# Performance work log

Hardware: AMD Instinct MI355X
Metric: run time of the kernel (lower is better)

Reference implementation:

```python
import jax, jax.numpy as jnp
import numpy as np

N = 100000
K = 27  # 3^3 kernel offsets for dimension=3
EPS = 1e-6


def layer_norm(x, gamma, beta):
    mu = jnp.mean(x, axis=-1, keepdims=True)
    var = jnp.mean(jnp.square(x - mu), axis=-1, keepdims=True)
    return (x - mu) * jax.lax.rsqrt(var + EPS) * gamma + beta


def sparse_conv3(x, idx, mask, W):
    # gather-GEMM-scatter form of Minkowski sparse conv:
    # x: [N, Cin], idx/mask: [N, K], W: [K, Cin, Cout]
    xg = jnp.where(mask[..., None], x[idx], 0.0)  # [N, K, Cin]
    return jnp.einsum('nkc,kcd->nd', xg, W)


def setup_inputs() -> dict:
    key = jax.random.key(0)
    ks = jax.random.split(key, 6)
    x = jax.random.normal(ks[0], (N, 32), dtype=jnp.float32)
    neighbor_idx = jax.random.randint(ks[1], (N, K), 0, N, dtype=jnp.int32)
    neighbor_mask = jax.random.randint(ks[2], (N, K), 0, 2) > 0
    W_conv = jax.random.normal(ks[3], (32, 32), dtype=jnp.float32) * 0.1
    W1 = jax.random.normal(ks[4], (K, 32, 128), dtype=jnp.float32) * 0.05
    W2 = jax.random.normal(ks[5], (K, 128, 32), dtype=jnp.float32) * 0.05
    return {
        'x': x,
        'neighbor_idx': neighbor_idx,
        'neighbor_mask': neighbor_mask,
        'W_conv': W_conv,
        'gamma0': jnp.ones((32,), jnp.float32),
        'beta0': jnp.zeros((32,), jnp.float32),
        'W1': W1,
        'gamma1': jnp.ones((128,), jnp.float32),
        'beta1': jnp.zeros((128,), jnp.float32),
        'W2': W2,
        'gamma2': jnp.ones((32,), jnp.float32),
        'beta2': jnp.zeros((32,), jnp.float32),
    }


def reference(x, neighbor_idx, neighbor_mask, W_conv, gamma0, beta0,
              W1, gamma1, beta1, W2, gamma2, beta2):
    gelu = lambda t: jax.nn.gelu(t, approximate=False)  # torch default (erf)
    residual = x
    out = x @ W_conv                      # kernel_size=1 conv == dense matmul
    out = gelu(layer_norm(out, gamma0, beta0))
    out = sparse_conv3(out, neighbor_idx, neighbor_mask, W1)
    out = gelu(layer_norm(out, gamma1, beta1))
    out = sparse_conv3(out, neighbor_idx, neighbor_mask, W2)
    out = layer_norm(out, gamma2, beta2)
    out = out + residual
    return gelu(out)
```

## Files before the change

kernel.cpp:

```cpp
#include <hip/hip_runtime.h>
#include <hip/hip_bf16.h>
#include <math.h>

#define NPTS 100000
#define KOFF 27

typedef __attribute__((ext_vector_type(8))) __bf16 bf16x8;
typedef __attribute__((ext_vector_type(4))) float f32x4;

__device__ __forceinline__ unsigned short f2bf(float f) {
    unsigned int u = __float_as_uint(f);
    u += 0x7fffu + ((u >> 16) & 1u);
    return (unsigned short)(u >> 16);
}

__device__ __forceinline__ float gelu_erf(float v) {
    return 0.5f * v * (1.0f + erff(v * 0.70710678118654752f));
}

__global__ __launch_bounds__(256)
void repack_kernel(const float* __restrict__ W1, const float* __restrict__ W2,
                   const void* __restrict__ maskp,
                   unsigned short* __restrict__ W1p,
                   unsigned short* __restrict__ W2p,
                   int* __restrict__ flagp) {
    int o = blockIdx.x * 256 + threadIdx.x;
    if (o == 0) {
        const unsigned int* mw = (const unsigned int*)maskp;
        int f = 0;
        for (int i = 0; i < 64; ++i) f |= (mw[i] > 1u) ? 1 : 0;
        *flagp = f;
    }
    if (o < KOFF * 32 * 128) {
        int j = o & 7, lane = (o >> 3) & 63;
        int quad = lane >> 4, nn = lane & 15;
        int ct1 = (o >> 9) & 7, k1 = o >> 12;
        int kk1 = quad * 8 + j;
        W1p[o] = f2bf(W1[(k1 * 32 + kk1) * 128 + (ct1 * 16 + nn)]);
        int ct2 = (o >> 9) & 1, kc2 = (o >> 10) & 3, k2 = o >> 12;
        int kk2 = kc2 * 32 + quad * 8 + j;
        W2p[o] = f2bf(W2[(k2 * 128 + kk2) * 32 + (ct2 * 16 + nn)]);
    }
}

__global__ __launch_bounds__(256)
void conv1_ln_gelu(const float* __restrict__ x, const float* __restrict__ Wc,
                   const float* __restrict__ g0, const float* __restrict__ b0,
                   unsigned short* __restrict__ out0) {
    __shared__ float xs[256];
    __shared__ float wc[1024];
    int t = threadIdx.x;
    int nb = blockIdx.x * 8;
    xs[t] = x[nb * 32 + t];
    for (int i = t; i < 1024; i += 256) wc[i] = Wc[i];
    __syncthreads();
    int r = t >> 5, d = t & 31;
    const float* xr = &xs[r * 32];
    float v = 0.f;
#pragma unroll
    for (int c = 0; c < 32; ++c) v = fmaf(xr[c], wc[c * 32 + d], v);
    float s = v, s2 = v * v;
#pragma unroll
    for (int m = 16; m >= 1; m >>= 1) {
        s  += __shfl_xor(s,  m, 32);
        s2 += __shfl_xor(s2, m, 32);
    }
    float mu  = s * (1.f / 32.f);
    float var = s2 * (1.f / 32.f) - mu * mu;
    float y = (v - mu) * rsqrtf(var + 1e-6f) * g0[d] + b0[d];
    out0[nb * 32 + t] = f2bf(gelu_erf(y));
}

__device__ __forceinline__ void stage_gidx64(int* s_gidx, const int* nidx,
                                             const void* maskp, int mflag,
                                             int nb, int t) {
    int cnt = (NPTS - nb < 64 ? NPTS - nb : 64) * KOFF;
    for (int i = t; i < 64 * KOFF; i += 64) {
        int g = -1;
        if (i < cnt) {
            int gi = nidx[nb * KOFF + i];
            int m = mflag ? (int)((const unsigned char*)maskp)[nb * KOFF + i]
                          : ((const int*)maskp)[nb * KOFF + i];
            g = m ? gi : -1;
        }
        s_gidx[i] = g;
    }
}

__global__ __launch_bounds__(64, 2)
void conv_k1(const int* __restrict__ nidx, const void* __restrict__ maskp,
             const int* __restrict__ flagp,
             const unsigned short* __restrict__ out0,
             const unsigned short* __restrict__ W1p,
             const float* __restrict__ g1, const float* __restrict__ b1,
             unsigned short* __restrict__ out1) {
    __shared__ int s_gidx[64 * KOFF];

    int t = threadIdx.x;
    int nb = blockIdx.x * 64;
    int mflag = *flagp;
    stage_gidx64(s_gidx, nidx, maskp, mflag, nb, t);
    __syncthreads();

    int lane = t & 63;
    int mrow = lane & 15, quad = lane >> 4;
    const unsigned short* a_base = out0 + quad * 8;
    const int* gp0 = &s_gidx[(0 * 16 + mrow) * KOFF];
    const int* gp1 = &s_gidx[(1 * 16 + mrow) * KOFF];
    const int* gp2 = &s_gidx[(2 * 16 + mrow) * KOFF];
    const int* gp3 = &s_gidx[(3 * 16 + mrow) * KOFF];

    f32x4 acc[4][8] = {};
    bf16x8 a[2][4], b[2][8];

    {
        const unsigned short* wb = W1p + (lane << 3);
#pragma unroll
        for (int ct = 0; ct < 8; ++ct)
            b[0][ct] = *reinterpret_cast<const bf16x8*>(wb + ((ct * 64) << 3));
        int g0 = gp0[0], g1i = gp1[0], g2 = gp2[0], g3 = gp3[0];
        a[0][0] = bf16x8{}; if (g0  >= 0) a[0][0] = *reinterpret_cast<const bf16x8*>(a_base + g0  * 32);
        a[0][1] = bf16x8{}; if (g1i >= 0) a[0][1] = *reinterpret_cast<const bf16x8*>(a_base + g1i * 32);
        a[0][2] = bf16x8{}; if (g2  >= 0) a[0][2] = *reinterpret_cast<const bf16x8*>(a_base + g2  * 32);
        a[0][3] = bf16x8{}; if (g3  >= 0) a[0][3] = *reinterpret_cast<const bf16x8*>(a_base + g3  * 32);
    }

#pragma unroll
    for (int k = 0; k < KOFF; ++k) {
        int cur = k & 1, nxt = cur ^ 1;
        if (k + 1 < KOFF) {
            const unsigned short* wb = W1p + ((((k + 1) * 8) * 64 + lane) << 3);
#pragma unroll
            for (int ct = 0; ct < 8; ++ct)
                b[nxt][ct] = *reinterpret_cast<const bf16x8*>(wb + ((ct * 64) << 3));
            int g0 = gp0[k + 1], g1i = gp1[k + 1], g2 = gp2[k + 1], g3 = gp3[k + 1];
            a[nxt][0] = bf16x8{}; if (g0  >= 0) a[nxt][0] = *reinterpret_cast<const bf16x8*>(a_base + g0  * 32);
            a[nxt][1] = bf16x8{}; if (g1i >= 0) a[nxt][1] = *reinterpret_cast<const bf16x8*>(a_base + g1i * 32);
            a[nxt][2] = bf16x8{}; if (g2  >= 0) a[nxt][2] = *reinterpret_cast<const bf16x8*>(a_base + g2  * 32);
            a[nxt][3] = bf16x8{}; if (g3  >= 0) a[nxt][3] = *reinterpret_cast<const bf16x8*>(a_base + g3  * 32);
        }
#pragma unroll
        for (int rt = 0; rt < 4; ++rt)
#pragma unroll
            for (int ct = 0; ct < 8; ++ct)
                acc[rt][ct] = __builtin_amdgcn_mfma_f32_16x16x32_bf16(a[cur][rt], b[cur][ct], acc[rt][ct], 0, 0, 0);
    }

    float gv[8], bv[8];
#pragma unroll
    for (int ct = 0; ct < 8; ++ct) {
        gv[ct] = g1[ct * 16 + mrow];
        bv[ct] = b1[ct * 16 + mrow];
    }
#pragma unroll
    for (int rt = 0; rt < 4; ++rt) {
        int n_base = nb + rt * 16 + quad * 4;
#pragma unroll
        for (int r = 0; r < 4; ++r) {
            float s = 0.f, s2 = 0.f;
#pragma unroll
            for (int ct = 0; ct < 8; ++ct) { float v = acc[rt][ct][r]; s += v; s2 += v * v; }
#pragma unroll
            for (int m = 1; m <= 8; m <<= 1) {
                s  += __shfl_xor(s,  m, 16);
                s2 += __shfl_xor(s2, m, 16);
            }
            float mu = s * (1.f / 128.f);
            float rs = rsqrtf(s2 * (1.f / 128.f) - mu * mu + 1e-6f);
            int n = n_base + r;
            if (n < NPTS) {
#pragma unroll
                for (int ct = 0; ct < 8; ++ct) {
                    float y = (acc[rt][ct][r] - mu) * rs * gv[ct] + bv[ct];
                    out1[n * 128 + ct * 16 + mrow] = f2bf(gelu_erf(y));
                }
            }
        }
    }
}

__global__ __launch_bounds__(64, 2)
void conv_k2(const int* __restrict__ nidx, const void* __restrict__ maskp,
             const int* __restrict__ flagp,
             const unsigned short* __restrict__ out1,
             const unsigned short* __restrict__ W2p,
             const float* __restrict__ g2, const float* __restrict__ b2,
             const float* __restrict__ x, float* __restrict__ outp) {
    __shared__ int s_gidx[64 * KOFF];

    int t = threadIdx.x;
    int nb = blockIdx.x * 64;
    int mflag = *flagp;
    stage_gidx64(s_gidx, nidx, maskp, mflag, nb, t);
    __syncthreads();

    int lane = t & 63;
    int mrow = lane & 15, quad = lane >> 4;
    const unsigned short* a_base = out1 + quad * 8;
    const int* gp0 = &s_gidx[(0 * 16 + mrow) * KOFF];
    const int* gp1 = &s_gidx[(1 * 16 + mrow) * KOFF];
    const int* gp2 = &s_gidx[(2 * 16 + mrow) * KOFF];
    const int* gp3 = &s_gidx[(3 * 16 + mrow) * KOFF];

    f32x4 acc[4][2] = {};
    bf16x8 a[2][4][4], b[2][8];

    {
        const unsigned short* wb = W2p + (lane << 3);
#pragma unroll
        for (int f = 0; f < 8; ++f)
            b[0][f] = *reinterpret_cast<const bf16x8*>(wb + ((f * 64) << 3));
        int gg[4] = { gp0[0], gp1[0], gp2[0], gp3[0] };
#pragma unroll
        for (int rt = 0; rt < 4; ++rt) {
#pragma unroll
            for (int kc = 0; kc < 4; ++kc) a[0][rt][kc] = bf16x8{};
            if (gg[rt] >= 0) {
#pragma unroll
                for (int kc = 0; kc < 4; ++kc)
                    a[0][rt][kc] = *reinterpret_cast<const bf16x8*>(a_base + gg[rt] * 128 + kc * 32);
            }
        }
    }

#pragma unroll
    for (int k = 0; k < KOFF; ++k) {
        int cur = k & 1, nxt = cur ^ 1;
        if (k + 1 < KOFF) {
            const unsigned short* wb = W2p + ((((k + 1) * 8) * 64 + lane) << 3);
#pragma unroll
            for (int f = 0; f < 8; ++f)
                b[nxt][f] = *reinterpret_cast<const bf16x8*>(wb + ((f * 64) << 3));
            int gg[4] = { gp0[k + 1], gp1[k + 1], gp2[k + 1], gp3[k + 1] };
#pragma unroll
            for (int rt = 0; rt < 4; ++rt) {
#pragma unroll
                for (int kc = 0; kc < 4; ++kc) a[nxt][rt][kc] = bf16x8{};
                if (gg[rt] >= 0) {
#pragma unroll
                    for (int kc = 0; kc < 4; ++kc)
                        a[nxt][rt][kc] = *reinterpret_cast<const bf16x8*>(a_base + gg[rt] * 128 + kc * 32);
                }
            }
        }
#pragma unroll
        for (int rt = 0; rt < 4; ++rt)
#pragma unroll
            for (int kc = 0; kc < 4; ++kc) {
                acc[rt][0] = __builtin_amdgcn_mfma_f32_16x16x32_bf16(a[cur][rt][kc], b[cur][kc * 2 + 0], acc[rt][0], 0, 0, 0);
                acc[rt][1] = __builtin_amdgcn_mfma_f32_16x16x32_bf16(a[cur][rt][kc], b[cur][kc * 2 + 1], acc[rt][1], 0, 0, 0);
            }
    }

    float gv0 = g2[mrow], gv1 = g2[mrow + 16];
    float bv0 = b2[mrow], bv1 = b2[mrow + 16];
#pragma unroll
    for (int rt = 0; rt < 4; ++rt) {
        int n_base = nb + rt * 16 + quad * 4;
#pragma unroll
        for (int r = 0; r < 4; ++r) {
            float v0 = acc[rt][0][r], v1 = acc[rt][1][r];
            float s = v0 + v1, s2 = v0 * v0 + v1 * v1;
#pragma unroll
            for (int m = 1; m <= 8; m <<= 1) {
                s  += __shfl_xor(s,  m, 16);
                s2 += __shfl_xor(s2, m, 16);
            }
            float mu = s * (1.f / 32.f);
            float rs = rsqrtf(s2 * (1.f / 32.f) - mu * mu + 1e-6f);
            int n = n_base + r;
            if (n < NPTS) {
                float y0 = (v0 - mu) * rs * gv0 + bv0 + x[n * 32 + mrow];
                float y1 = (v1 - mu) * rs * gv1 + bv1 + x[n * 32 + mrow + 16];
                outp[n * 32 + mrow]      = gelu_erf(y0);
                outp[n * 32 + mrow + 16] = gelu_erf(y1);
            }
        }
    }
}

extern "C" void kernel_launch(void* const* d_in, const int* in_sizes, int n_in,
                              void* d_out, int out_size, void* d_ws, size_t ws_size,
                              hipStream_t stream) {
    const float* x    = (const float*)d_in[0];
    const int*   nidx = (const int*)d_in[1];
    const void*  maskp = d_in[2];
    const float* Wc = (const float*)d_in[3];
    const float* g0 = (const float*)d_in[4];
    const float* b0 = (const float*)d_in[5];
    const float* W1 = (const float*)d_in[6];
    const float* g1 = (const float*)d_in[7];
    const float* b1 = (const float*)d_in[8];
    const float* W2 = (const float*)d_in[9];
    const float* g2 = (const float*)d_in[10];
    const float* b2 = (const float*)d_in[11];

    char* ws = (char*)d_ws;
    unsigned short* out0 = (unsigned short*)ws;
    unsigned short* out1 = (unsigned short*)(ws + 6400000);
    unsigned short* W1p  = (unsigned short*)(ws + 32000000);
    unsigned short* W2p  = W1p + KOFF * 32 * 128;
    int* flagp = (int*)(W2p + KOFF * 128 * 32);

    repack_kernel<<<432, 256, 0, stream>>>(W1, W2, maskp, W1p, W2p, flagp);
    conv1_ln_gelu<<<NPTS / 8, 256, 0, stream>>>(x, Wc, g0, b0, out0);
    conv_k1<<<(NPTS + 63) / 64, 64, 0, stream>>>(nidx, maskp, flagp, out0, W1p, g1, b1, out1);
    conv_k2<<<(NPTS + 63) / 64, 64, 0, stream>>>(nidx, maskp, flagp, out1, W2p, g2, b2, x, (float*)d_out);
}
```

Baseline: 276.9 us.

## Stage conv_k2 gathered rows through LDS with compacted coalesced neighbor loads

conv_k2 now builds, per kernel offset, a compacted list of valid neighbor indices. Each neighbor's 256-byte row is fetched cooperatively by 16 lanes as contiguous 16-byte loads into a padded, double-buffered LDS staging area. MFMA A-fragments are then read from LDS through a per-row slot byte, and masked rows point to a zeroed slot. This aims to coalesce the random row gathers and skip loads for masked neighbors. The cost is extra LDS, setup passes and barriers, and the launch-bounds occupancy hint is dropped. There is no synchronisation between the LDS staging writes and the reads of other lanes, which is only safe because a single-wave block runs in lockstep.

```diff
diff --git a/kernel.cpp b/kernel.cpp
--- a/kernel.cpp
+++ b/kernel.cpp
@@ -7,6 +7,7 @@
 
 typedef __attribute__((ext_vector_type(8))) __bf16 bf16x8;
 typedef __attribute__((ext_vector_type(4))) float f32x4;
+typedef __attribute__((ext_vector_type(4))) int i32x4;
 
 __device__ __forceinline__ unsigned short f2bf(float f) {
     unsigned int u = __float_as_uint(f);
@@ -179,7 +180,10 @@
     }
 }
 
-__global__ __launch_bounds__(64, 2)
+#define SLOT_STRIDE 272
+#define BUF_SZ (65 * SLOT_STRIDE)
+
+__global__ __launch_bounds__(64)
 void conv_k2(const int* __restrict__ nidx, const void* __restrict__ maskp,
              const int* __restrict__ flagp,
              const unsigned short* __restrict__ out1,
@@ -187,69 +191,95 @@
              const float* __restrict__ g2, const float* __restrict__ b2,
              const float* __restrict__ x, float* __restrict__ outp) {
     __shared__ int s_gidx[64 * KOFF];
+    __shared__ int glist[KOFF][64];
+    __shared__ unsigned char sbyte[KOFF][64];
+    __shared__ unsigned int cpb[KOFF][16];
+    __shared__ __align__(16) char stage[2 * BUF_SZ];
 
     int t = threadIdx.x;
     int nb = blockIdx.x * 64;
     int mflag = *flagp;
+
     stage_gidx64(s_gidx, nidx, maskp, mflag, nb, t);
-    __syncthreads();
-
-    int lane = t & 63;
-    int mrow = lane & 15, quad = lane >> 4;
-    const unsigned short* a_base = out1 + quad * 8;
-    const int* gp0 = &s_gidx[(0 * 16 + mrow) * KOFF];
-    const int* gp1 = &s_gidx[(1 * 16 + mrow) * KOFF];
-    const int* gp2 = &s_gidx[(2 * 16 + mrow) * KOFF];
-    const int* gp3 = &s_gidx[(3 * 16 + mrow) * KOFF];
-
+    if (t < 34) {
+        int buf = (t >= 17) ? 1 : 0, c = (t >= 17) ? t - 17 : t;
+        *reinterpret_cast<i32x4*>(stage + buf * BUF_SZ + 64 * SLOT_STRIDE + c * 16) = i32x4{0, 0, 0, 0};
+    }
+    __syncthreads();
+
+    if (t < KOFF) {
+        int c = 0;
+        for (int r = 0; r < 64; ++r) {
+            int g = s_gidx[r * KOFF + t];
+            unsigned char sb = 64;
+            if (g >= 0) { sb = (unsigned char)c; glist[t][c] = g; ++c; }
+            sbyte[t][r] = sb;
+        }
+        for (int p = c; p < 64; ++p) glist[t][p] = 0;
+    }
+    __syncthreads();
+    for (int i = t; i < KOFF * 16; i += 64) {
+        int k = i >> 4, mr = i & 15;
+        cpb[k][mr] = (unsigned)sbyte[k][mr]
+                   | ((unsigned)sbyte[k][16 + mr] << 8)
+                   | ((unsigned)sbyte[k][32 + mr] << 16)
+                   | ((unsigned)sbyte[k][48 + mr] << 24);
+    }
+    __syncthreads();
+
+    int mrow = t & 15, quad = t >> 4;
+    int sub = t >> 4, q = t & 15;
     f32x4 acc[4][2] = {};
-    bf16x8 a[2][4][4], b[2][8];
+    i32x4 sreg[16];
+    bf16x8 breg[2][8];
 
     {
-        const unsigned short* wb = W2p + (lane << 3);
+#pragma unroll
+        for (int j = 0; j < 16; ++j) {
+            int g = glist[0][4 * j + sub];
+            sreg[j] = *reinterpret_cast<const i32x4*>(out1 + (size_t)g * 128 + q * 8);
+        }
+        const unsigned short* wb = W2p + (t << 3);
 #pragma unroll
         for (int f = 0; f < 8; ++f)
-            b[0][f] = *reinterpret_cast<const bf16x8*>(wb + ((f * 64) << 3));
-        int gg[4] = { gp0[0], gp1[0], gp2[0], gp3[0] };
-#pragma unroll
-        for (int rt = 0; rt < 4; ++rt) {
-#pragma unroll
-            for (int kc = 0; kc < 4; ++kc) a[0][rt][kc] = bf16x8{};
-            if (gg[rt] >= 0) {
-#pragma unroll
-                for (int kc = 0; kc < 4; ++kc)
-                    a[0][rt][kc] = *reinterpret_cast<const bf16x8*>(a_base + gg[rt] * 128 + kc * 32);
-            }
-        }
+            breg[0][f] = *reinterpret_cast<const bf16x8*>(wb + ((f * 64) << 3));
+#pragma unroll
+        for (int j = 0; j < 16; ++j)
+            *reinterpret_cast<i32x4*>(stage + (4 * j + sub) * SLOT_STRIDE + q * 16) = sreg[j];
     }
 
 #pragma unroll
     for (int k = 0; k < KOFF; ++k) {
         int cur = k & 1, nxt = cur ^ 1;
         if (k + 1 < KOFF) {
-            const unsigned short* wb = W2p + ((((k + 1) * 8) * 64 + lane) << 3);
+#pragma unroll
+            for (int j = 0; j < 16; ++j) {
+                int g = glist[k + 1][4 * j + sub];
+                sreg[j] = *reinterpret_cast<const i32x4*>(out1 + (size_t)g * 128 + q * 8);
+            }
+            const unsigned short* wb = W2p + ((((k + 1) * 8) * 64 + t) << 3);
 #pragma unroll
             for (int f = 0; f < 8; ++f)
-                b[nxt][f] = *reinterpret_cast<const bf16x8*>(wb + ((f * 64) << 3));
-            int gg[4] = { gp0[k + 1], gp1[k + 1], gp2[k + 1], gp3[k + 1] };
-#pragma unroll
-            for (int rt = 0; rt < 4; ++rt) {
-#pragma unroll
-                for (int kc = 0; kc < 4; ++kc) a[nxt][rt][kc] = bf16x8{};
-                if (gg[rt] >= 0) {
-#pragma unroll
-                    for (int kc = 0; kc < 4; ++kc)
-                        a[nxt][rt][kc] = *reinterpret_cast<const bf16x8*>(a_base + gg[rt] * 128 + kc * 32);
-                }
-            }
-        }
-#pragma unroll
-        for (int rt = 0; rt < 4; ++rt)
+                breg[nxt][f] = *reinterpret_cast<const bf16x8*>(wb + ((f * 64) << 3));
+        }
+        unsigned wm = cpb[k][mrow];
+        const char* base = stage + cur * BUF_SZ + quad * 16;
+#pragma unroll
+        for (int rt = 0; rt < 4; ++rt) {
+            int s = (wm >> (8 * rt)) & 255;
+            const char* rowb = base + s * SLOT_STRIDE;
 #pragma unroll
             for (int kc = 0; kc < 4; ++kc) {
-                acc[rt][0] = __builtin_amdgcn_mfma_f32_16x16x32_bf16(a[cur][rt][kc], b[cur][kc * 2 + 0], acc[rt][0], 0, 0, 0);
-                acc[rt][1] = __builtin_amdgcn_mfma_f32_16x16x32_bf16(a[cur][rt][kc], b[cur][kc * 2 + 1], acc[rt][1], 0, 0, 0);
-            }
+                bf16x8 af = *reinterpret_cast<const bf16x8*>(rowb + kc * 64);
+                acc[rt][0] = __builtin_amdgcn_mfma_f32_16x16x32_bf16(af, breg[cur][kc * 2 + 0], acc[rt][0], 0, 0, 0);
+                acc[rt][1] = __builtin_amdgcn_mfma_f32_16x16x32_bf16(af, breg[cur][kc * 2 + 1], acc[rt][1], 0, 0, 0);
+            }
+        }
+        if (k + 1 < KOFF) {
+#pragma unroll
+            for (int j = 0; j < 16; ++j)
+                *reinterpret_cast<i32x4*>(stage + nxt * BUF_SZ + (4 * j + sub) * SLOT_STRIDE + q * 16) = sreg[j];
+        }
     }
 
     float gv0 = g2[mrow], gv1 = g2[mrow + 16];
```

After: 520.8 us. 88.1% more time.

## Split sparse conv blocks across two waves and deepen gather prefetch

Applied to the files above, without the earlier changes.

Both sparse-conv kernels now launch 128 threads per 64-point block, with each wave owning 32 rows instead of one wave owning all 64. This halves per-wave accumulator and A-fragment registers so more waves can fit per CU, at the cost of each wave reloading the full weight slice. conv_k1 also gets a triple-buffered gather that prefetches two offsets ahead, and conv_k2 issues the gather loads before the weight loads. The index-staging loop now strides by 128 so the two waves share that work.

```diff
diff --git a/kernel.cpp b/kernel.cpp
--- a/kernel.cpp
+++ b/kernel.cpp
@@ -71,11 +71,11 @@
     out0[nb * 32 + t] = f2bf(gelu_erf(y));
 }
 
-__device__ __forceinline__ void stage_gidx64(int* s_gidx, const int* nidx,
-                                             const void* maskp, int mflag,
-                                             int nb, int t) {
+__device__ __forceinline__ void stage_gidx128(int* s_gidx, const int* nidx,
+                                              const void* maskp, int mflag,
+                                              int nb, int t) {
     int cnt = (NPTS - nb < 64 ? NPTS - nb : 64) * KOFF;
-    for (int i = t; i < 64 * KOFF; i += 64) {
+    for (int i = t; i < 64 * KOFF; i += 128) {
         int g = -1;
         if (i < cnt) {
             int gi = nidx[nb * KOFF + i];
@@ -87,7 +87,7 @@
     }
 }
 
-__global__ __launch_bounds__(64, 2)
+__global__ __launch_bounds__(128, 3)
 void conv_k1(const int* __restrict__ nidx, const void* __restrict__ maskp,
              const int* __restrict__ flagp,
              const unsigned short* __restrict__ out0,
@@ -99,51 +99,50 @@
     int t = threadIdx.x;
     int nb = blockIdx.x * 64;
     int mflag = *flagp;
-    stage_gidx64(s_gidx, nidx, maskp, mflag, nb, t);
+    stage_gidx128(s_gidx, nidx, maskp, mflag, nb, t);
     __syncthreads();
 
-    int lane = t & 63;
+    int lane = t & 63, w = t >> 6;
     int mrow = lane & 15, quad = lane >> 4;
     const unsigned short* a_base = out0 + quad * 8;
-    const int* gp0 = &s_gidx[(0 * 16 + mrow) * KOFF];
-    const int* gp1 = &s_gidx[(1 * 16 + mrow) * KOFF];
-    const int* gp2 = &s_gidx[(2 * 16 + mrow) * KOFF];
-    const int* gp3 = &s_gidx[(3 * 16 + mrow) * KOFF];
-
-    f32x4 acc[4][8] = {};
-    bf16x8 a[2][4], b[2][8];
+    const int* gp0 = &s_gidx[(w * 32 + 0 * 16 + mrow) * KOFF];
+    const int* gp1 = &s_gidx[(w * 32 + 1 * 16 + mrow) * KOFF];
+
+    f32x4 acc[2][8] = {};
+    bf16x8 a[3][2], b[2][8];
 
     {
         const unsigned short* wb = W1p + (lane << 3);
 #pragma unroll
         for (int ct = 0; ct < 8; ++ct)
             b[0][ct] = *reinterpret_cast<const bf16x8*>(wb + ((ct * 64) << 3));
-        int g0 = gp0[0], g1i = gp1[0], g2 = gp2[0], g3 = gp3[0];
+        int g0 = gp0[0], g1i = gp1[0];
         a[0][0] = bf16x8{}; if (g0  >= 0) a[0][0] = *reinterpret_cast<const bf16x8*>(a_base + g0  * 32);
         a[0][1] = bf16x8{}; if (g1i >= 0) a[0][1] = *reinterpret_cast<const bf16x8*>(a_base + g1i * 32);
-        a[0][2] = bf16x8{}; if (g2  >= 0) a[0][2] = *reinterpret_cast<const bf16x8*>(a_base + g2  * 32);
-        a[0][3] = bf16x8{}; if (g3  >= 0) a[0][3] = *reinterpret_cast<const bf16x8*>(a_base + g3  * 32);
+        g0 = gp0[1]; g1i = gp1[1];
+        a[1][0] = bf16x8{}; if (g0  >= 0) a[1][0] = *reinterpret_cast<const bf16x8*>(a_base + g0  * 32);
+        a[1][1] = bf16x8{}; if (g1i >= 0) a[1][1] = *reinterpret_cast<const bf16x8*>(a_base + g1i * 32);
     }
 
 #pragma unroll
     for (int k = 0; k < KOFF; ++k) {
-        int cur = k & 1, nxt = cur ^ 1;
         if (k + 1 < KOFF) {
             const unsigned short* wb = W1p + ((((k + 1) * 8) * 64 + lane) << 3);
 #pragma unroll
             for (int ct = 0; ct < 8; ++ct)
-                b[nxt][ct] = *reinterpret_cast<const bf16x8*>(wb + ((ct * 64) << 3));
-            int g0 = gp0[k + 1], g1i = gp1[k + 1], g2 = gp2[k + 1], g3 = gp3[k + 1];
-            a[nxt][0] = bf16x8{}; if (g0  >= 0) a[nxt][0] = *reinterpret_cast<const bf16x8*>(a_base + g0  * 32);
-            a[nxt][1] = bf16x8{}; if (g1i >= 0) a[nxt][1] = *reinterpret_cast<const bf16x8*>(a_base + g1i * 32);
-            a[nxt][2] = bf16x8{}; if (g2  >= 0) a[nxt][2] = *reinterpret_cast<const bf16x8*>(a_base + g2  * 32);
-            a[nxt][3] = bf16x8{}; if (g3  >= 0) a[nxt][3] = *reinterpret_cast<const bf16x8*>(a_base + g3  * 32);
-        }
-#pragma unroll
-        for (int rt = 0; rt < 4; ++rt)
+                b[(k + 1) & 1][ct] = *reinterpret_cast<const bf16x8*>(wb + ((ct * 64) << 3));
+        }
+        if (k + 2 < KOFF) {
+            int g0 = gp0[k + 2], g1i = gp1[k + 2];
+            int s = (k + 2) % 3;
+            a[s][0] = bf16x8{}; if (g0  >= 0) a[s][0] = *reinterpret_cast<const bf16x8*>(a_base + g0  * 32);
+            a[s][1] = bf16x8{}; if (g1i >= 0) a[s][1] = *reinterpret_cast<const bf16x8*>(a_base + g1i * 32);
+        }
+#pragma unroll
+        for (int rt = 0; rt < 2; ++rt)
 #pragma unroll
             for (int ct = 0; ct < 8; ++ct)
-                acc[rt][ct] = __builtin_amdgcn_mfma_f32_16x16x32_bf16(a[cur][rt], b[cur][ct], acc[rt][ct], 0, 0, 0);
+                acc[rt][ct] = __builtin_amdgcn_mfma_f32_16x16x32_bf16(a[k % 3][rt], b[k & 1][ct], acc[rt][ct], 0, 0, 0);
     }
 
     float gv[8], bv[8];
@@ -153,8 +152,8 @@
         bv[ct] = b1[ct * 16 + mrow];
     }
 #pragma unroll
-    for (int rt = 0; rt < 4; ++rt) {
-        int n_base = nb + rt * 16 + quad * 4;
+    for (int rt = 0; rt < 2; ++rt) {
+        int n_base = nb + w * 32 + rt * 16 + quad * 4;
 #pragma unroll
         for (int r = 0; r < 4; ++r) {
             float s = 0.f, s2 = 0.f;
@@ -179,7 +178,7 @@
     }
 }
 
-__global__ __launch_bounds__(64, 2)
+__global__ __launch_bounds__(128, 3)
 void conv_k2(const int* __restrict__ nidx, const void* __restrict__ maskp,
              const int* __restrict__ flagp,
              const unsigned short* __restrict__ out1,
@@ -191,49 +190,43 @@
     int t = threadIdx.x;
     int nb = blockIdx.x * 64;
     int mflag = *flagp;
-    stage_gidx64(s_gidx, nidx, maskp, mflag, nb, t);
+    stage_gidx128(s_gidx, nidx, maskp, mflag, nb, t);
     __syncthreads();
 
-    int lane = t & 63;
+    int lane = t & 63, w = t >> 6;
     int mrow = lane & 15, quad = lane >> 4;
     const unsigned short* a_base = out1 + quad * 8;
-    const int* gp0 = &s_gidx[(0 * 16 + mrow) * KOFF];
-    const int* gp1 = &s_gidx[(1 * 16 + mrow) * KOFF];
-    const int* gp2 = &s_gidx[(2 * 16 + mrow) * KOFF];
-    const int* gp3 = &s_gidx[(3 * 16 + mrow) * KOFF];
-
-    f32x4 acc[4][2] = {};
-    bf16x8 a[2][4][4], b[2][8];
+    const int* gp0 = &s_gidx[(w * 32 + 0 * 16 + mrow) * KOFF];
+    const int* gp1 = &s_gidx[(w * 32 + 1 * 16 + mrow) * KOFF];
+
+    f32x4 acc[2][2] = {};
+    bf16x8 a[2][2][4], b[2][8];
 
     {
+        int gg[2] = { gp0[0], gp1[0] };
+#pragma unroll
+        for (int rt = 0; rt < 2; ++rt) {
+#pragma unroll
+            for (int kc = 0; kc < 4; ++kc) a[0][rt][kc] = bf16x8{};
+            if (gg[rt] >= 0) {
+#pragma unroll
+                for (int kc = 0; kc < 4; ++kc)
+                    a[0][rt][kc] = *reinterpret_cast<const bf16x8*>(a_base + gg[rt] * 128 + kc * 32);
+            }
+        }
         const unsigned short* wb = W2p + (lane << 3);
 #pragma unroll
         for (int f = 0; f < 8; ++f)
             b[0][f] = *reinterpret_cast<const bf16x8*>(wb + ((f * 64) << 3));
-        int gg[4] = { gp0[0], gp1[0], gp2[0], gp3[0] };
-#pragma unroll
-        for (int rt = 0; rt < 4; ++rt) {
-#pragma unroll
-            for (int kc = 0; kc < 4; ++kc) a[0][rt][kc] = bf16x8{};
-            if (gg[rt] >= 0) {
-#pragma unroll
-                for (int kc = 0; kc < 4; ++kc)
-                    a[0][rt][kc] = *reinterpret_cast<const bf16x8*>(a_base + gg[rt] * 128 + kc * 32);
-            }
-        }
     }
 
 #pragma unroll
     for (int k = 0; k < KOFF; ++k) {
         int cur = k & 1, nxt = cur ^ 1;
         if (k + 1 < KOFF) {
-            const unsigned short* wb = W2p + ((((k + 1) * 8) * 64 + lane) << 3);
-#pragma unroll
-            for (int f = 0; f < 8; ++f)
-                b[nxt][f] = *reinterpret_cast<const bf16x8*>(wb + ((f * 64) << 3));
-            int gg[4] = { gp0[k + 1], gp1[k + 1], gp2[k + 1], gp3[k + 1] };
-#pragma unroll
-            for (int rt = 0; rt < 4; ++rt) {
+            int gg[2] = { gp0[k + 1], gp1[k + 1] };
+#pragma unroll
+            for (int rt = 0; rt < 2; ++rt) {
 #pragma unroll
                 for (int kc = 0; kc < 4; ++kc) a[nxt][rt][kc] = bf16x8{};
                 if (gg[rt] >= 0) {
@@ -242,9 +235,13 @@
                         a[nxt][rt][kc] = *reinterpret_cast<const bf16x8*>(a_base + gg[rt] * 128 + kc * 32);
                 }
             }
-        }
-#pragma unroll
-        for (int rt = 0; rt < 4; ++rt)
+            const unsigned short* wb = W2p + ((((k + 1) * 8) * 64 + lane) << 3);
+#pragma unroll
+            for (int f = 0; f < 8; ++f)
+                b[nxt][f] = *reinterpret_cast<const bf16x8*>(wb + ((f * 64) << 3));
+        }
+#pragma unroll
+        for (int rt = 0; rt < 2; ++rt)
 #pragma unroll
             for (int kc = 0; kc < 4; ++kc) {
                 acc[rt][0] = __builtin_amdgcn_mfma_f32_16x16x32_bf16(a[cur][rt][kc], b[cur][kc * 2 + 0], acc[rt][0], 0, 0, 0);
@@ -255,8 +252,8 @@
     float gv0 = g2[mrow], gv1 = g2[mrow + 16];
     float bv0 = b2[mrow], bv1 = b2[mrow + 16];
 #pragma unroll
-    for (int rt = 0; rt < 4; ++rt) {
-        int n_base = nb + rt * 16 + quad * 4;
+    for (int rt = 0; rt < 2; ++rt) {
+        int n_base = nb + w * 32 + rt * 16 + quad * 4;
 #pragma unroll
         for (int r = 0; r < 4; ++r) {
             float v0 = acc[rt][0][r], v1 = acc[rt][1][r];
@@ -304,6 +301,6 @@
 
     repack_kernel<<<432, 256, 0, stream>>>(W1, W2, maskp, W1p, W2p, flagp);
     conv1_ln_gelu<<<NPTS / 8, 256, 0, stream>>>(x, Wc, g0, b0, out0);
-    conv_k1<<<(NPTS + 63) / 64, 64, 0, stream>>>(nidx, maskp, flagp, out0, W1p, g1, b1, out1);
-    conv_k2<<<(NPTS + 63) / 64, 64, 0, stream>>>(nidx, maskp, flagp, out1, W2p, g2, b2, x, (float*)d_out);
-}
+    conv_k1<<<(NPTS + 63) / 64, 128, 0, stream>>>(nidx, maskp, flagp, out0, W1p, g1, b1, out1);
+    conv_k2<<<(NPTS + 63) / 64, 128, 0, stream>>>(nidx, maskp, flagp, out1, W2p, g2, b2, x, (float*)d_out);
+}
```

Result: slower. 330.3 us (+19.3%).

## Split second sparse conv into dense per-offset GEMM then gather-sum

Applied to the files above, without the earlier changes.

Reorders the second sparse conv so that each point's 128-channel feature is first multiplied by all 27 offset weights, writing a 27×N×32 bf16 intermediate. A separate gather kernel then sums the 27 neighbour rows of 32 channels and applies LayerNorm, residual and GELU. This replaces gathering 128-wide rows per neighbour with gathering 32-wide rows, at the cost of writing and reading roughly 173 MB of intermediate and one more kernel launch. The old fused kernel is kept as a fallback for when the workspace is too small.

```diff
diff --git a/kernel.cpp b/kernel.cpp
--- a/kernel.cpp
+++ b/kernel.cpp
@@ -180,12 +180,152 @@
 }
 
 __global__ __launch_bounds__(64, 2)
-void conv_k2(const int* __restrict__ nidx, const void* __restrict__ maskp,
-             const int* __restrict__ flagp,
-             const unsigned short* __restrict__ out1,
-             const unsigned short* __restrict__ W2p,
-             const float* __restrict__ g2, const float* __restrict__ b2,
-             const float* __restrict__ x, float* __restrict__ outp) {
+void gemm_tmp(const unsigned short* __restrict__ out1,
+              const unsigned short* __restrict__ W2p,
+              unsigned short* __restrict__ tmp) {
+    int t = threadIdx.x;
+    int nb = blockIdx.x * 64;
+    int mrow = t & 15, quad = t >> 4;
+
+    bf16x8 a[4][4];
+#pragma unroll
+    for (int rt = 0; rt < 4; ++rt) {
+        int n = nb + rt * 16 + mrow;
+        bool ok = (n < NPTS);
+#pragma unroll
+        for (int kc = 0; kc < 4; ++kc) {
+            a[rt][kc] = bf16x8{};
+            if (ok)
+                a[rt][kc] = *reinterpret_cast<const bf16x8*>(out1 + (size_t)n * 128 + kc * 32 + quad * 8);
+        }
+    }
+    bf16x8 b[2][8];
+    {
+        const unsigned short* wb = W2p + (t << 3);
+#pragma unroll
+        for (int f = 0; f < 8; ++f)
+            b[0][f] = *reinterpret_cast<const bf16x8*>(wb + ((f * 64) << 3));
+    }
+
+#pragma unroll
+    for (int k = 0; k < KOFF; ++k) {
+        int cur = k & 1, nxt = cur ^ 1;
+        if (k + 1 < KOFF) {
+            const unsigned short* wb = W2p + ((((k + 1) * 8) * 64 + t) << 3);
+#pragma unroll
+            for (int f = 0; f < 8; ++f)
+                b[nxt][f] = *reinterpret_cast<const bf16x8*>(wb + ((f * 64) << 3));
+        }
+        f32x4 acc[4][2] = {};
+#pragma unroll
+        for (int rt = 0; rt < 4; ++rt)
+#pragma unroll
+            for (int kc = 0; kc < 4; ++kc) {
+                acc[rt][0] = __builtin_amdgcn_mfma_f32_16x16x32_bf16(a[rt][kc], b[cur][kc * 2 + 0], acc[rt][0], 0, 0, 0);
+                acc[rt][1] = __builtin_amdgcn_mfma_f32_16x16x32_bf16(a[rt][kc], b[cur][kc * 2 + 1], acc[rt][1], 0, 0, 0);
+            }
+        unsigned short* tk = tmp + (size_t)k * NPTS * 32;
+#pragma unroll
+        for (int rt = 0; rt < 4; ++rt) {
+            int n0 = nb + rt * 16 + quad * 4;
+#pragma unroll
+            for (int r = 0; r < 4; ++r) {
+                int n = n0 + r;
+                if (n < NPTS) {
+#pragma unroll
+                    for (int ct = 0; ct < 2; ++ct)
+                        tk[(size_t)n * 32 + ct * 16 + mrow] = f2bf(acc[rt][ct][r]);
+                }
+            }
+        }
+    }
+}
+
+__global__ __launch_bounds__(256)
+void gather_sum(const int* __restrict__ nidx, const void* __restrict__ maskp,
+                const int* __restrict__ flagp,
+                const unsigned short* __restrict__ tmp,
+                const float* __restrict__ g2, const float* __restrict__ b2,
+                const float* __restrict__ x, float* __restrict__ outp) {
+    __shared__ int s_gidx[64 * KOFF];
+    int t = threadIdx.x;
+    int nb = blockIdx.x * 64;
+    int mflag = *flagp;
+    int cnt = (NPTS - nb < 64 ? NPTS - nb : 64) * KOFF;
+    for (int i = t; i < 64 * KOFF; i += 256) {
+        int g = -1;
+        if (i < cnt) {
+            int gi = nidx[nb * KOFF + i];
+            int m = mflag ? (int)((const unsigned char*)maskp)[nb * KOFF + i]
+                          : ((const int*)maskp)[nb * KOFF + i];
+            g = m ? gi : -1;
+        }
+        s_gidx[i] = g;
+    }
+    __syncthreads();
+
+    int rl = t >> 2, q = t & 3;
+    const int* gp = &s_gidx[rl * KOFF];
+    const unsigned short* tq = tmp + q * 8;
+
+    float acc[8] = {};
+    uint4 ring[3];
+#pragma unroll
+    for (int d = 0; d < 3; ++d) {
+        int g = gp[d];
+        ring[d] = uint4{0u, 0u, 0u, 0u};
+        if (g >= 0)
+            ring[d] = *reinterpret_cast<const uint4*>(tq + ((size_t)d * NPTS + g) * 32);
+    }
+#pragma unroll
+    for (int k = 0; k < KOFF; ++k) {
+        uint4 v = ring[k % 3];
+        if (k + 3 < KOFF) {
+            int g = gp[k + 3];
+            ring[k % 3] = uint4{0u, 0u, 0u, 0u};
+            if (g >= 0)
+                ring[k % 3] = *reinterpret_cast<const uint4*>(tq + ((size_t)(k + 3) * NPTS + g) * 32);
+        }
+        unsigned int w0 = v.x, w1 = v.y, w2 = v.z, w3 = v.w;
+        acc[0] += __uint_as_float(w0 << 16);
+        acc[1] += __uint_as_float(w0 & 0xffff0000u);
+        acc[2] += __uint_as_float(w1 << 16);
+        acc[3] += __uint_as_float(w1 & 0xffff0000u);
+        acc[4] += __uint_as_float(w2 << 16);
+        acc[5] += __uint_as_float(w2 & 0xffff0000u);
+        acc[6] += __uint_as_float(w3 << 16);
+        acc[7] += __uint_as_float(w3 & 0xffff0000u);
+    }
+
+    float s = 0.f, s2 = 0.f;
+#pragma unroll
+    for (int j = 0; j < 8; ++j) { s += acc[j]; s2 += acc[j] * acc[j]; }
+    s += __shfl_xor(s, 1); s2 += __shfl_xor(s2, 1);
+    s += __shfl_xor(s, 2); s2 += __shfl_xor(s2, 2);
+    float mu = s * (1.f / 32.f);
+    float rs = rsqrtf(s2 * (1.f / 32.f) - mu * mu + 1e-6f);
+
+    int n = nb + rl;
+    if (n < NPTS) {
+        float o[8];
+#pragma unroll
+        for (int j = 0; j < 8; ++j) {
+            int c = q * 8 + j;
+            float y = (acc[j] - mu) * rs * g2[c] + b2[c] + x[n * 32 + c];
+            o[j] = gelu_erf(y);
+        }
+        *reinterpret_cast<float4*>(outp + n * 32 + q * 8)     = make_float4(o[0], o[1], o[2], o[3]);
+        *reinterpret_cast<float4*>(outp + n * 32 + q * 8 + 4) = make_float4(o[4], o[5], o[6], o[7]);
+    }
+}
+
+__global__ __launch_bounds__(64, 2)
+void conv_k2_fb(const int* __restrict__ nidx, const void* __restrict__ maskp,
+                const int* __restrict__ flagp,
+                const unsigned short* __restrict__ out1,
+                const unsigned short* __restrict__ W2p,
+                const float* __restrict__ g2, const float* __restrict__ b2,
+                const float* __restrict__ x, float* __restrict__ outp) {
     __shared__ int s_gidx[64 * KOFF];
 
     int t = threadIdx.x;
@@ -218,7 +358,7 @@
             if (gg[rt] >= 0) {
 #pragma unroll
                 for (int kc = 0; kc < 4; ++kc)
-                    a[0][rt][kc] = *reinterpret_cast<const bf16x8*>(a_base + gg[rt] * 128 + kc * 32);
+                    a[0][rt][kc] = *reinterpret_cast<const bf16x8*>(a_base + (size_t)gg[rt] * 128 + kc * 32);
             }
         }
     }
@@ -239,7 +379,7 @@
                 if (gg[rt] >= 0) {
 #pragma unroll
                     for (int kc = 0; kc < 4; ++kc)
-                        a[nxt][rt][kc] = *reinterpret_cast<const bf16x8*>(a_base + gg[rt] * 128 + kc * 32);
+                        a[nxt][rt][kc] = *reinterpret_cast<const bf16x8*>(a_base + (size_t)gg[rt] * 128 + kc * 32);
                 }
             }
         }
@@ -299,11 +439,18 @@
     unsigned short* out0 = (unsigned short*)ws;
     unsigned short* out1 = (unsigned short*)(ws + 6400000);
     unsigned short* W1p  = (unsigned short*)(ws + 32000000);
-    unsigned short* W2p  = W1p + KOFF * 32 * 128;
-    int* flagp = (int*)(W2p + KOFF * 128 * 32);
+    unsigned short* W2p  = (unsigned short*)(ws + 32221184);
+    int* flagp           = (int*)(ws + 32442368);
+    unsigned short* tmp  = (unsigned short*)(ws + 32442432);
+    const size_t NEED_TMP = 32442432UL + (size_t)KOFF * NPTS * 32 * 2;
 
     repack_kernel<<<432, 256, 0, stream>>>(W1, W2, maskp, W1p, W2p, flagp);
     conv1_ln_gelu<<<NPTS / 8, 256, 0, stream>>>(x, Wc, g0, b0, out0);
     conv_k1<<<(NPTS + 63) / 64, 64, 0, stream>>>(nidx, maskp, flagp, out0, W1p, g1, b1, out1);
-    conv_k2<<<(NPTS + 63) / 64, 64, 0, stream>>>(nidx, maskp, flagp, out1, W2p, g2, b2, x, (float*)d_out);
-}
+    if (ws_size >= NEED_TMP) {
+        gemm_tmp<<<(NPTS + 63) / 64, 64, 0, stream>>>(out1, W2p, tmp);
+        gather_sum<<<(NPTS + 63) / 64, 256, 0, stream>>>(nidx, maskp, flagp, tmp, g2, b2, x, (float*)d_out);
+    } else {
+        conv_k2_fb<<<(NPTS + 63) / 64, 64, 0, stream>>>(nidx, maskp, flagp, out1, W2p, g2, b2, x, (float*)d_out);
+    }
+}
```

Result: no change. 277.8 us (+0.3%).
